# Kernel optimization log

Measured on AMD Instinct MI355X. Metric: run time of the kernel, lower is better.

The kernel has to match this reference:

```python
import jax, jax.numpy as jnp
import numpy as np

HEAD_DIM = 64
SELECT = 256  # number of selected rows/cols (m)
NUM_ITER = 4  # Newton-Schulz iterations


def _select_idx(T, mask, m):
    # top-k over sum of features (select_type='sum'), done under stop_gradient (torch.no_grad)
    somme = jax.lax.stop_gradient(jnp.sum(T, axis=-1))  # [B,H,N]
    neg = -jnp.finfo(somme.dtype).max
    somme = jnp.where(mask[:, None, :], somme, neg)
    _, idx = jax.lax.top_k(somme, m)  # [B,H,m], descending like argsort(descending=True)[:m]
    return idx


def _gather_rows(T, idx):
    # T: [B,H,N,D], idx: [B,H,m] -> [B,H,m,D]  (index_select over flattened (b h n))
    return jnp.take_along_axis(T, idx[..., None], axis=2)


def _iterative_inv(mat, num_iter):
    m = mat.shape[-1]
    I = jnp.eye(m, dtype=mat.dtype)
    K = mat
    # V0 = K^T / max_j(sum_i K_ij)
    scale = 1.0 / jnp.max(jnp.sum(K, axis=-2), axis=-1)[:, :, None, None]
    V = scale * jnp.swapaxes(K, -1, -2)
    for _ in range(num_iter):
        KV = jnp.matmul(K, V)
        V = jnp.matmul(0.25 * V, 13.0 * I - jnp.matmul(KV, 15.0 * I - jnp.matmul(KV, 7.0 * I - KV)))
    return V


def setup_inputs() -> dict:
    key = jax.random.key(0)
    kq, kk, kv = jax.random.split(key, 3)
    B, H, N, D = 2, 8, 4096, HEAD_DIM
    Q = jax.random.normal(kq, (B, H, N, D), dtype=jnp.float32)
    K = jax.random.normal(kk, (B, H, N, D), dtype=jnp.float32)
    V = jax.random.normal(kv, (B, H, N, D), dtype=jnp.float32)
    mask = jnp.ones((B, N), dtype=bool)
    return {"Q": Q, "K": K, "V": V, "mask": mask}


def reference(Q, K, V, mask):
    m = SELECT
    Qs = Q / np.sqrt(HEAD_DIM).astype(np.float32)
    # select_mode='default' -> index_select_different: indices for K from K, for Q from (scaled) Q
    idx_k = _select_idx(K, mask, m)
    idx_q = _select_idx(Qs, mask, m)
    nc = _gather_rows(K, idx_k)   # [B,H,m,D] selected columns (from K)
    nr = _gather_rows(Qs, idx_k := idx_q if False else idx_q) if False else _gather_rows(Qs, idx_q)  # [B,H,m,D]
    c = jnp.einsum('bhnd,bhmd->bhnm', Qs, nc)   # [B,H,N,m]
    r = jnp.einsum('bhmd,bhnd->bhmn', nr, K)    # [B,H,m,N]
    neg = -jnp.finfo(Qs.dtype).max
    r = jnp.where(mask[:, None, None, :], r, neg)
    kernel_1 = jax.nn.softmax(c, axis=-1)                 # [B,H,N,m]
    u = _gather_rows(kernel_1, idx_q)                     # [B,H,m,m]
    kernel_3 = jax.nn.softmax(r, axis=-1)                 # [B,H,m,N]
    kernel_2_inv = _iterative_inv(u, NUM_ITER)            # [B,H,m,m]
    RV = jnp.matmul(kernel_3, V)                          # [B,H,m,D]
    X = jnp.matmul(kernel_1, jnp.matmul(kernel_2_inv, RV))  # [B,H,N,D]
    return X
```

## Files before the change

### kernel.cpp

```cpp
#include <hip/hip_runtime.h>
#include <float.h>


#define G    16
#define NSEQ 4096
#define DH   64
#define MSEL 256
#define NSL  16

typedef __attribute__((ext_vector_type(8))) short short8;
typedef __attribute__((ext_vector_type(4))) float floatx4;
typedef __attribute__((ext_vector_type(4))) unsigned short ushort4v;
typedef unsigned short ush;

static __device__ __forceinline__ ush f2b(float x) {
    union { float f; unsigned u; } c{x};
    unsigned r = c.u + 0x7FFFu + ((c.u >> 16) & 1u);
    return (ush)(r >> 16);
}
static __device__ __forceinline__ float b2f(ush h) {
    union { unsigned u; float f; } c{(unsigned)h << 16};
    return c.f;
}
static __device__ __forceinline__ void split_store(ush* __restrict__ h, ush* __restrict__ l,
                                                   int off, float4 v, float scale) {
    float a0 = v.x * scale, a1 = v.y * scale, a2 = v.z * scale, a3 = v.w * scale;
    ush h0 = f2b(a0), h1 = f2b(a1), h2 = f2b(a2), h3 = f2b(a3);
    ushort4v hv = { h0, h1, h2, h3 };
    ushort4v lv = { f2b(a0 - b2f(h0)), f2b(a1 - b2f(h1)), f2b(a2 - b2f(h2)), f2b(a3 - b2f(h3)) };
    *(ushort4v*)&h[off] = hv;
    *(ushort4v*)&l[off] = lv;
}
static __device__ __forceinline__ floatx4 mfma3(short8 ah, short8 al, short8 bh, short8 bl, floatx4 acc) {
    acc = __builtin_amdgcn_mfma_f32_16x16x32_bf16(al, bh, acc, 0, 0, 0);
    acc = __builtin_amdgcn_mfma_f32_16x16x32_bf16(ah, bl, acc, 0, 0, 0);
    acc = __builtin_amdgcn_mfma_f32_16x16x32_bf16(ah, bh, acc, 0, 0, 0);
    return acc;
}

__global__ __launch_bounds__(256) void rowsum_kernel(const float* __restrict__ Q, const float* __restrict__ K,
                                                     float* __restrict__ sumQ, float* __restrict__ sumK,
                                                     float* __restrict__ k2) {
    long row = (long)blockIdx.x * 16 + (threadIdx.x >> 4);
    int c4 = (threadIdx.x & 15) * 4;
    float4 q = *(const float4*)(Q + row * DH + c4);
    float4 k = *(const float4*)(K + row * DH + c4);
    float qs = q.x + q.y + q.z + q.w;
    float ks = k.x + k.y + k.z + k.w;
    float k2s = k.x * k.x + k.y * k.y + k.z * k.z + k.w * k.w;
#pragma unroll
    for (int off = 8; off; off >>= 1) {
        qs += __shfl_xor(qs, off); ks += __shfl_xor(ks, off); k2s += __shfl_xor(k2s, off);
    }
    if ((threadIdx.x & 15) == 0) { sumQ[row] = qs; sumK[row] = ks; k2[row] = k2s; }
}

__global__ __launch_bounds__(256) void topk_select(const float* __restrict__ sumQ, const float* __restrict__ sumK,
                                                   int* __restrict__ idxQ, int* __restrict__ idxK,
                                                   const float* __restrict__ k2, float* __restrict__ Kmax2,
                                                   float* __restrict__ colsum) {
    __shared__ unsigned red[4];
    __shared__ float redf[4];
    __shared__ unsigned eqpre[64];
    __shared__ unsigned cnt_sel;
    int g = blockIdx.x, which = blockIdx.y;
    const float* s = (which ? sumK : sumQ) + (long)g * NSEQ;
    int* out = (which ? idxK : idxQ) + g * MSEL;
    int t = threadIdx.x, lane = t & 63, wid = t >> 6;
    if (which == 0) colsum[g * 256 + t] = 0.f;
    unsigned k[16];
#pragma unroll
    for (int i = 0; i < 16; i++) {
        unsigned u = __float_as_uint(s[t + 256 * i]);
        k[i] = (u & 0x80000000u) ? ~u : (u | 0x80000000u);
    }
    unsigned T = 0;
    for (int b = 31; b >= 0; b--) {
        unsigned trial = T | (1u << b);
        int c = 0;
#pragma unroll
        for (int i = 0; i < 16; i++) c += (k[i] >= trial);
#pragma unroll
        for (int off = 32; off; off >>= 1) c += __shfl_xor(c, off);
        __syncthreads();
        if (lane == 0) red[wid] = (unsigned)c;
        __syncthreads();
        unsigned tot = red[0] + red[1] + red[2] + red[3];
        if (tot == MSEL) { T = trial; break; }
        if (tot > MSEL) T = trial;
    }
    int cg = 0;
#pragma unroll
    for (int i = 0; i < 16; i++) cg += (k[i] > T);
#pragma unroll
    for (int off = 32; off; off >>= 1) cg += __shfl_xor(cg, off);
    __syncthreads();
    if (lane == 0) red[wid] = (unsigned)cg;
    if (t == 0) cnt_sel = 0;
    __syncthreads();
    unsigned ngreater = red[0] + red[1] + red[2] + red[3];
    unsigned want_eq = MSEL - ngreater;
#pragma unroll
    for (int i = 0; i < 16; i++) {
        unsigned long long be = __ballot(k[i] == T);
        if (lane == 0) eqpre[i * 4 + wid] = (unsigned)__popcll(be);
    }
    __syncthreads();
    if (t == 0) {
        unsigned run = 0;
        for (int j = 0; j < 64; j++) { unsigned c = eqpre[j]; eqpre[j] = run; run += c; }
    }
    __syncthreads();
#pragma unroll
    for (int i = 0; i < 16; i++) {
        int idx = t + 256 * i;
        unsigned long long lt = (1ull << lane) - 1;
        bool gt = (k[i] > T);
        unsigned long long bg = __ballot(gt);
        unsigned wbase = 0;
        if (lane == 0) wbase = atomicAdd(&cnt_sel, (unsigned)__popcll(bg));
        wbase = __shfl((int)wbase, 0);
        if (gt) out[wbase + __popcll(bg & lt)] = idx;
        bool eq = (k[i] == T);
        unsigned long long be = __ballot(eq);
        if (eq) {
            unsigned rank = eqpre[i * 4 + wid] + (unsigned)__popcll(be & lt);
            if (rank < want_eq) out[ngreater + rank] = idx;
        }
    }
    if (which == 1) {
        float mx = 0.f;
#pragma unroll
        for (int i = 0; i < 16; i++) mx = fmaxf(mx, k2[(long)g * NSEQ + t + 256 * i]);
#pragma unroll
        for (int off = 32; off; off >>= 1) mx = fmaxf(mx, __shfl_xor(mx, off));
        __syncthreads();
        if (lane == 0) redf[wid] = mx;
        __syncthreads();
        if (t == 0) Kmax2[g] = fmaxf(fmaxf(redf[0], redf[1]), fmaxf(redf[2], redf[3]));
    }
}

__global__ __launch_bounds__(256) void gather_kernel(const float* __restrict__ Q, const float* __restrict__ K,
                                                     const int* __restrict__ idxQ, const int* __restrict__ idxK,
                                                     const float* __restrict__ Kmax2,
                                                     float* __restrict__ nr,
                                                     ush* __restrict__ ncH, ush* __restrict__ ncL,
                                                     float* __restrict__ Mb) {
    int wid = threadIdx.x >> 6, lane = threadIdx.x & 63;
    long t = (long)blockIdx.x * 4 + wid;
    long g = t >> 8;
    int iq = idxQ[t], ik = idxK[t];
    float qv = Q[(g * NSEQ + iq) * DH + lane] * 0.125f;
    nr[t * DH + lane] = qv;
    float kv = K[(g * NSEQ + ik) * DH + lane];
    ush h = f2b(kv);
    ncH[t * DH + lane] = h;
    ncL[t * DH + lane] = f2b(kv - b2f(h));
    float n2 = qv * qv;
#pragma unroll
    for (int off = 32; off; off >>= 1) n2 += __shfl_xor(n2, off);
    if (lane == 0) Mb[t] = sqrtf(n2 * Kmax2[g]);
}

__global__ __launch_bounds__(256, 4) void flash_rv(const float* __restrict__ nr, const float* __restrict__ K,
                                                   const float* __restrict__ V, const float* __restrict__ Mb,
                                                   float* __restrict__ Lp, float* __restrict__ RVp) {
    __shared__ __align__(16) ush B1h[64 * 72];
    __shared__ __align__(16) ush B1l[64 * 72];
    __shared__ __align__(16) ush Ph[64 * 72];
    __shared__ float msh[64];
    __shared__ float lred[64][2];
    int ns = blockIdx.x, s = blockIdx.y, g = blockIdx.z;
    int t = threadIdx.x, lane = t & 63, w = t >> 6;
    int wr = w >> 1, wc = w & 1, ml = lane & 15, quad = lane >> 4;
    int lr = t >> 2, lq = t & 3;
    const float* nrg = nr + (long)g * 16384 + (long)s * 64 * 64;
    const float* Kg  = K + (long)g * 262144 + (long)ns * 256 * 64;
    const float* Vg  = V + (long)g * 262144 + (long)ns * 256 * 64;
    short8 Ah[2][2], Al[2][2];
// ... 180 lines not shown
    __syncthreads();
    if (MODE == 1) {
        float invL[4][4];
#pragma unroll
        for (int i = 0; i < 4; i++)
#pragma unroll
            for (int r = 0; r < 4; r++) invL[i][r] = 1.0f / Lr[16 * i + quad * 4 + r];
        float* ug = Out + (long)g * 65536 + (long)strip * 64 * 256;
#pragma unroll
        for (int i = 0; i < 4; i++)
#pragma unroll
            for (int r = 0; r < 4; r++) {
                int row = 16 * i + quad * 4 + r;
#pragma unroll
                for (int c = 0; c < 4; c++)
                    ug[(long)row * 256 + c * 64 + w * 16 + ml] = sacc[c][i][r] * invL[i][r];
            }
#pragma unroll
        for (int c = 0; c < 4; c++) {
            float v = 0.f;
#pragma unroll
            for (int i = 0; i < 4; i++)
#pragma unroll
                for (int r = 0; r < 4; r++) v += sacc[c][i][r] * invL[i][r];
            v += __shfl_xor(v, 16);
            v += __shfl_xor(v, 32);
            if (quad == 0) atomicAdd(&colsum[g * 256 + c * 64 + w * 16 + ml], v);
        }
        return;
    }
    floatx4 xacc[2][2] = {};
    const ush* wHg = WtH + (long)g * 16384;
    const ush* wLg = WtL + (long)g * 16384;
#pragma unroll
    for (int h = 0; h < 4; h++) {
        __syncthreads();
#pragma unroll
        for (int i = 0; i < 4; i++)
#pragma unroll
            for (int r = 0; r < 4; r++) {
                int row = 16 * i + quad * 4 + r;
                float p = sacc[h][i][r];
                ush hh = f2b(p);
                Ph[row * 72 + w * 16 + ml] = hh;
                Pl[row * 72 + w * 16 + ml] = f2b(p - b2f(hh));
            }
        {
            const ush* sH = wHg + lr * 256 + h * 64;
            const ush* sL = wLg + lr * 256 + h * 64;
            *(uint4*)&Wh[lr * 72 + lq * 8]       = *(const uint4*)&sH[lq * 8];
            *(uint4*)&Wh[lr * 72 + (lq + 4) * 8] = *(const uint4*)&sH[(lq + 4) * 8];
            *(uint4*)&Wl[lr * 72 + lq * 8]       = *(const uint4*)&sL[lq * 8];
            *(uint4*)&Wl[lr * 72 + (lq + 4) * 8] = *(const uint4*)&sL[(lq + 4) * 8];
        }
        __syncthreads();
#pragma unroll
        for (int kq = 0; kq < 2; kq++) {
            short8 a0h = *(const short8*)&Ph[(wr * 32 + ml) * 72 + kq * 32 + quad * 8];
            short8 a0l = *(const short8*)&Pl[(wr * 32 + ml) * 72 + kq * 32 + quad * 8];
            short8 a1h = *(const short8*)&Ph[(wr * 32 + 16 + ml) * 72 + kq * 32 + quad * 8];
            short8 a1l = *(const short8*)&Pl[(wr * 32 + 16 + ml) * 72 + kq * 32 + quad * 8];
            short8 b0h = *(const short8*)&Wh[(wc * 32 + ml) * 72 + kq * 32 + quad * 8];
            short8 b0l = *(const short8*)&Wl[(wc * 32 + ml) * 72 + kq * 32 + quad * 8];
            short8 b1h = *(const short8*)&Wh[(wc * 32 + 16 + ml) * 72 + kq * 32 + quad * 8];
            short8 b1l = *(const short8*)&Wl[(wc * 32 + 16 + ml) * 72 + kq * 32 + quad * 8];
            xacc[0][0] = mfma3(a0h, a0l, b0h, b0l, xacc[0][0]);
            xacc[0][1] = mfma3(a0h, a0l, b1h, b1l, xacc[0][1]);
            xacc[1][0] = mfma3(a1h, a1l, b0h, b0l, xacc[1][0]);
            xacc[1][1] = mfma3(a1h, a1l, b1h, b1l, xacc[1][1]);
        }
    }
    float* outg = Out + (long)g * 262144 + (long)strip * 64 * 64;
#pragma unroll
    for (int i2 = 0; i2 < 2; i2++)
#pragma unroll
        for (int j2 = 0; j2 < 2; j2++)
#pragma unroll
            for (int r = 0; r < 4; r++) {
                int row = wr * 32 + i2 * 16 + quad * 4 + r;
                outg[(long)row * 64 + wc * 32 + j2 * 16 + ml] = xacc[i2][j2][r] / Lr[row];
            }
}

__global__ __launch_bounds__(256) void mergeprep_kernel(const float* __restrict__ Lp, const float* __restrict__ RVp,
                                                        ush* __restrict__ RVt,
                                                        const float* __restrict__ u, const float* __restrict__ colsum,
                                                        ush* __restrict__ u_bf, ush* __restrict__ V0,
                                                        float* __restrict__ scale) {
    __shared__ float tile[64][65];
    __shared__ float smax[4];
    int g = blockIdx.y;
    int t = threadIdx.x, lane = t & 63, wid = t >> 6;
    if (blockIdx.z == 0) {
        int s = blockIdx.x >> 2, mq = blockIdx.x & 3;
        int d = t & 63;
        int m0 = mq * 16 + (t >> 6) * 4;
        long pb = ((long)(g * 4 + s)) * NSL;
#pragma unroll
        for (int mm = 0; mm < 4; mm++) {
            int rho = m0 + mm;
            float L = 0.f, val = 0.f;
#pragma unroll
            for (int n = 0; n < NSL; n++) {
                L   += Lp[(pb + n) * 64 + rho];
                val += RVp[(pb + n) * 4096 + rho * 64 + d];
            }
            RVt[(long)g * 16384 + d * 256 + s * 64 + rho] = f2b(val / L);
        }
        return;
    }
    int tc = blockIdx.x & 3, tr = (blockIdx.x >> 2) & 3;
    float v = colsum[g * 256 + t];
#pragma unroll
    for (int off = 32; off; off >>= 1) v = fmaxf(v, __shfl_xor(v, off));
    if (lane == 0) smax[wid] = v;
    __syncthreads();
    float sc = 1.0f / fmaxf(fmaxf(smax[0], smax[1]), fmaxf(smax[2], smax[3]));
    if (t == 0 && tr == 0 && tc == 0) scale[g] = sc;
    long base = (long)g * MSEL * MSEL;
    const float* ug = u + base;
    int cq = (t & 15) * 4, r0 = t >> 4;
#pragma unroll
    for (int i = 0; i < 4; i++) {
        int r = r0 + 16 * i;
        float4 vv = *(const float4*)&ug[(long)(tr * 64 + r) * MSEL + tc * 64 + cq];
        long o = base + (long)(tr * 64 + r) * MSEL + tc * 64 + cq;
        ushort4v ub = { f2b(vv.x), f2b(vv.y), f2b(vv.z), f2b(vv.w) };
        *(ushort4v*)&u_bf[o] = ub;
        tile[r][cq] = vv.x; tile[r][cq + 1] = vv.y; tile[r][cq + 2] = vv.z; tile[r][cq + 3] = vv.w;
    }
    __syncthreads();
#pragma unroll
    for (int i = 0; i < 4; i++) {
        int r = r0 + 16 * i;
        ushort4v o = { f2b(sc * tile[cq][r]), f2b(sc * tile[cq + 1][r]),
                       f2b(sc * tile[cq + 2][r]), f2b(sc * tile[cq + 3][r]) };
        *(ushort4v*)&V0[base + (long)(tc * 64 + r) * MSEL + tr * 64 + cq] = o;
    }
}

__global__ __launch_bounds__(256) void nsAC(const ush* __restrict__ A0, const ush* __restrict__ B0t,
                                            const ush* __restrict__ A1, const ush* __restrict__ B1t,
                                            ush* __restrict__ C0rm, ush* __restrict__ C0t,
                                            ush* __restrict__ C1rm,
                                            const float* __restrict__ scale, int whichBase) {
    const int LD = 136;
    __shared__ __align__(16) ush As[64 * LD];
    __shared__ __align__(16) ush Bs[64 * LD];
    int z = blockIdx.z, g = z & 15, which = (z >> 4) + whichBase;
    int tm = blockIdx.y, tn = blockIdx.x;
    long base = (long)g * 65536;
    const ush* Ag = (which ? A1 : A0) + base + (long)tm * 64 * 256;
    const ush* Bg = (which ? B1t : B0t) + base + (long)tn * 64 * 256;
    int t = threadIdx.x;
    int lr = t >> 2, lq = t & 3;
    int w = t >> 6, lane = t & 63;
    int wr = w >> 1, wc = w & 1;
    int ml = lane & 15, quad = lane >> 4;
    floatx4 acc[2][2] = {};
#pragma unroll
    for (int h = 0; h < 2; h++) {
        __syncthreads();
#pragma unroll
        for (int rr = 0; rr < 4; rr++) {
            int col = (lq + 4 * rr) * 8;
            *(uint4*)&As[lr * LD + col] = *(const uint4*)(Ag + lr * 256 + h * 128 + col);
            *(uint4*)&Bs[lr * LD + col] = *(const uint4*)(Bg + lr * 256 + h * 128 + col);
        }
        __syncthreads();
#pragma unroll
        for (int kq = 0; kq < 4; kq++) {
            int ko = kq * 32 + quad * 8;
            short8 a0 = *(const short8*)&As[(wr * 32 + ml) * LD + ko];
            short8 a1 = *(const short8*)&As[(wr * 32 + 16 + ml) * LD + ko];
            short8 b0 = *(const short8*)&Bs[(wc * 32 + ml) * LD + ko];
            short8 b1 = *(const short8*)&Bs[(wc * 32 + 16 + ml) * LD + ko];
            acc[0][0] = __builtin_amdgcn_mfma_f32_16x16x32_bf16(a0, b0, acc[0][0], 0, 0, 0);
            acc[0][1] = __builtin_amdgcn_mfma_f32_16x16x32_bf16(a0, b1, acc[0][1], 0, 0, 0);
            acc[1][0] = __builtin_amdgcn_mfma_f32_16x16x32_bf16(a1, b0, acc[1][0], 0, 0, 0);
            acc[1][1] = __builtin_amdgcn_mfma_f32_16x16x32_bf16(a1, b1, acc[1][1], 0, 0, 0);
        }
    }
    float sc = (which == 0 && scale) ? scale[g] : 1.0f;
    int rowb = tm * 64 + wr * 32, colb = tn * 64 + wc * 32;
#pragma unroll
    for (int i = 0; i < 2; i++) {
#pragma unroll
        for (int j = 0; j < 2; j++) {
            int col = colb + j * 16 + ml;
            int r0 = rowb + i * 16 + quad * 4;
            ush h[4];
#pragma unroll
            for (int r = 0; r < 4; r++) h[r] = f2b(acc[i][j][r] * sc);
            if (which == 0) {
#pragma unroll
                for (int r = 0; r < 4; r++) C0rm[base + (long)(r0 + r) * 256 + col] = h[r];
                ushort4v ht = { h[0], h[1], h[2], h[3] };
                *(ushort4v*)&C0t[base + (long)col * 256 + r0] = ht;
            } else {
#pragma unroll
                for (int r = 0; r < 4; r++) C1rm[base + (long)(r0 + r) * 256 + col] = h[r];
            }
        }
    }
}

template <bool FINAL>
__global__ __launch_bounds__(256) void nsB(const ush* __restrict__ S, const ush* __restrict__ Et,
                                           const ush* __restrict__ St,
                                           ush* __restrict__ Eo, ush* __restrict__ Eot,
                                           ush* __restrict__ Pt) {
    const int LD = 136;
    __shared__ __align__(16) ush As[64 * LD];
    __shared__ __align__(16) ush B1s[64 * LD];
    __shared__ __align__(16) ush B2s[64 * LD];
    int g = blockIdx.z, tm = blockIdx.y, tn = blockIdx.x;
    long base = (long)g * 65536;
    const ush* Ag  = S + base + (long)tm * 64 * 256;
    const ush* B1g = Et + base + (long)tn * 64 * 256;
    const ush* B2g = St + base + (long)tn * 64 * 256;
    int t = threadIdx.x;
    int lr = t >> 2, lq = t & 3;
    int w = t >> 6, lane = t & 63;
    int wr = w >> 1, wc = w & 1;
    int ml = lane & 15, quad = lane >> 4;
    floatx4 acc1[2][2] = {};
    floatx4 acc2[2][2] = {};
#pragma unroll
    for (int h = 0; h < 2; h++) {
        __syncthreads();
#pragma unroll
        for (int rr = 0; rr < 4; rr++) {
            int col = (lq + 4 * rr) * 8;
            *(uint4*)&As[lr * LD + col]  = *(const uint4*)(Ag + lr * 256 + h * 128 + col);
            *(uint4*)&B1s[lr * LD + col] = *(const uint4*)(B1g + lr * 256 + h * 128 + col);
            if (!FINAL) *(uint4*)&B2s[lr * LD + col] = *(const uint4*)(B2g + lr * 256 + h * 128 + col);
        }
        __syncthreads();
#pragma unroll
        for (int kq = 0; kq < 4; kq++) {
            int ko = kq * 32 + quad * 8;
            short8 a0 = *(const short8*)&As[(wr * 32 + ml) * LD + ko];
            short8 a1 = *(const short8*)&As[(wr * 32 + 16 + ml) * LD + ko];
            short8 b10 = *(const short8*)&B1s[(wc * 32 + ml) * LD + ko];
            short8 b11 = *(const short8*)&B1s[(wc * 32 + 16 + ml) * LD + ko];
            acc1[0][0] = __builtin_amdgcn_mfma_f32_16x16x32_bf16(a0, b10, acc1[0][0], 0, 0, 0);
            acc1[0][1] = __builtin_amdgcn_mfma_f32_16x16x32_bf16(a0, b11, acc1[0][1], 0, 0, 0);
            acc1[1][0] = __builtin_amdgcn_mfma_f32_16x16x32_bf16(a1, b10, acc1[1][0], 0, 0, 0);
            acc1[1][1] = __builtin_amdgcn_mfma_f32_16x16x32_bf16(a1, b11, acc1[1][1], 0, 0, 0);
            if (!FINAL) {
                short8 b20 = *(const short8*)&B2s[(wc * 32 + ml) * LD + ko];
                short8 b21 = *(const short8*)&B2s[(wc * 32 + 16 + ml) * LD + ko];
                acc2[0][0] = __builtin_amdgcn_mfma_f32_16x16x32_bf16(a0, b20, acc2[0][0], 0, 0, 0);
                acc2[0][1] = __builtin_amdgcn_mfma_f32_16x16x32_bf16(a0, b21, acc2[0][1], 0, 0, 0);
                acc2[1][0] = __builtin_amdgcn_mfma_f32_16x16x32_bf16(a1, b20, acc2[1][0], 0, 0, 0);
                acc2[1][1] = __builtin_amdgcn_mfma_f32_16x16x32_bf16(a1, b21, acc2[1][1], 0, 0, 0);
            }
        }
    }
    int rowb = tm * 64 + wr * 32, colb = tn * 64 + wc * 32;
#pragma unroll
    for (int i = 0; i < 2; i++) {
#pragma unroll
        for (int j = 0; j < 2; j++) {
            int col = colb + j * 16 + ml;
            int r0 = rowb + i * 16 + quad * 4;
            ushort4v et = *(const ushort4v*)&Et[base + (long)col * 256 + r0];
            ushort4v st = *(const ushort4v*)&St[base + (long)col * 256 + r0];
            ushort4v pv;
#pragma unroll
            for (int r = 0; r < 4; r++) {
                float e = b2f(et[r]), s = b2f(st[r]);
                float p = 0.25f * (((r0 + r == col) ? 13.0f : 0.0f) - 15.0f * e + 7.0f * s - acc1[i][j][r]);
                pv[r] = f2b(p);
            }
            *(ushort4v*)&Pt[base + (long)col * 256 + r0] = pv;
            if (!FINAL) {
                ush h[4];
#pragma unroll
                for (int r = 0; r < 4; r++) {
                    float e = b2f(et[r]), s = b2f(st[r]);
                    float en = 0.25f * (13.0f * e - 15.0f * s + 7.0f * acc1[i][j][r] - acc2[i][j][r]);
                    h[r] = f2b(en);
                }
#pragma unroll
                for (int r = 0; r < 4; r++) Eo[base + (long)(r0 + r) * 256 + col] = h[r];
                ushort4v ht = { h[0], h[1], h[2], h[3] };
                *(ushort4v*)&Eot[base + (long)col * 256 + r0] = ht;
            }
        }
    }
}

__global__ __launch_bounds__(256) void nsW(const ush* __restrict__ V4, const ush* __restrict__ RVt,
                                           ush* __restrict__ WtH, ush* __restrict__ WtL) {
    const int LD = 136;
    __shared__ __align__(16) ush As[64 * LD];
    __shared__ __align__(16) ush Bs[64 * LD];
    int g = blockIdx.z, tm = blockIdx.y;
    long base = (long)g * 65536;
    const ush* Ag = V4 + base + (long)tm * 64 * 256;
    const ush* Bg = RVt + (long)g * 16384;
    int t = threadIdx.x;
    int lr = t >> 2, lq = t & 3;
    int w = t >> 6, lane = t & 63;
    int wr = w >> 1, wc = w & 1;
    int ml = lane & 15, quad = lane >> 4;
    floatx4 acc[2][2] = {};
#pragma unroll
    for (int h = 0; h < 2; h++) {
        __syncthreads();
#pragma unroll
        for (int rr = 0; rr < 4; rr++) {
            int col = (lq + 4 * rr) * 8;
            *(uint4*)&As[lr * LD + col] = *(const uint4*)(Ag + lr * 256 + h * 128 + col);
            *(uint4*)&Bs[lr * LD + col] = *(const uint4*)(Bg + lr * 256 + h * 128 + col);
        }
        __syncthreads();
#pragma unroll
        for (int kq = 0; kq < 4; kq++) {
            int ko = kq * 32 + quad * 8;
            short8 a0 = *(const short8*)&As[(wr * 32 + ml) * LD + ko];
            short8 a1 = *(const short8*)&As[(wr * 32 + 16 + ml) * LD + ko];
            short8 b0 = *(const short8*)&Bs[(wc * 32 + ml) * LD + ko];
            short8 b1 = *(const short8*)&Bs[(wc * 32 + 16 + ml) * LD + ko];
            acc[0][0] = __builtin_amdgcn_mfma_f32_16x16x32_bf16(a0, b0, acc[0][0], 0, 0, 0);
            acc[0][1] = __builtin_amdgcn_mfma_f32_16x16x32_bf16(a0, b1, acc[0][1], 0, 0, 0);
            acc[1][0] = __builtin_amdgcn_mfma_f32_16x16x32_bf16(a1, b0, acc[1][0], 0, 0, 0);
            acc[1][1] = __builtin_amdgcn_mfma_f32_16x16x32_bf16(a1, b1, acc[1][1], 0, 0, 0);
        }
    }
    int rowb = tm * 64 + wr * 32, colb = wc * 32;
#pragma unroll
    for (int i = 0; i < 2; i++) {
#pragma unroll
        for (int j = 0; j < 2; j++) {
            int col = colb + j * 16 + ml;
            int r0 = rowb + i * 16 + quad * 4;
            ushort4v hv, lv;
#pragma unroll
            for (int r = 0; r < 4; r++) {
                float v = acc[i][j][r];
                ush h = f2b(v);
                hv[r] = h;
                lv[r] = f2b(v - b2f(h));
            }
            *(ushort4v*)&WtH[(long)g * 16384 + (long)col * 256 + r0] = hv;
            *(ushort4v*)&WtL[(long)g * 16384 + (long)col * 256 + r0] = lv;
        }
    }
}

extern "C" void kernel_launch(void* const* d_in, const int* in_sizes, int n_in,
                              void* d_out, int out_size, void* d_ws, size_t ws_size,
                              hipStream_t stream) {
    (void)in_sizes; (void)n_in; (void)out_size; (void)ws_size;
    const float* Q = (const float*)d_in[0];
    const float* K = (const float*)d_in[1];
    const float* V = (const float*)d_in[2];

    float* ws    = (float*)d_ws;
    float* sumQ  = ws;
    float* sumK  = sumQ + 65536;
    float* k2    = sumK + 65536;
    float* nr    = k2 + 65536;
    float* u     = nr + 262144;
    float* Mb    = u + 1048576;
    float* Kmax2 = Mb + 4096;
    float* scale = Kmax2 + 16;
    float* colsum= scale + 16 + 32;
    float* Lp    = colsum + 4096;
    float* RVp   = Lp + 65536;
    int* idxQ    = (int*)(RVp + 4194304);
    int* idxK    = idxQ + 4096;
    ush* ncH     = (ush*)(idxK + 4096);
    ush* ncL     = ncH + 262144;
    ush* WtH     = ncL + 262144;
    ush* WtL     = WtH + 262144;
    ush* RVt     = WtL + 262144;
    ush* u_bf    = RVt + 262144;
    ush* Vacc_a  = u_bf + 1048576;
    ush* Vacc_b  = Vacc_a + 1048576;
    ush* E_a     = Vacc_b + 1048576;
    ush* Et_a    = E_a + 1048576;
    ush* E_b     = Et_a + 1048576;
    ush* Et_b    = E_b + 1048576;
    ush* Sbuf    = Et_b + 1048576;
    ush* St      = Sbuf + 1048576;
    ush* Ptb     = St + 1048576;

    dim3 blk(256);

    hipLaunchKernelGGL(rowsum_kernel, dim3(G * NSEQ / 16), blk, 0, stream, Q, K, sumQ, sumK, k2);
    hipLaunchKernelGGL(topk_select, dim3(G, 2), blk, 0, stream, sumQ, sumK, idxQ, idxK, k2, Kmax2, colsum);
    hipLaunchKernelGGL(gather_kernel, dim3(G * MSEL / 4), blk, 0, stream, Q, K, idxQ, idxK, Kmax2, nr, ncH, ncL, Mb);

    hipLaunchKernelGGL(flash_rv, dim3(NSL, 4, G), blk, 0, stream, nr, K, V, Mb, Lp, RVp);

    hipLaunchKernelGGL((fused_cx<1>), dim3(4, G), blk, 0, stream, nr, ncH, ncL,
                       (const ush*)0, (const ush*)0, u, colsum, 1.0f);

    hipLaunchKernelGGL(mergeprep_kernel, dim3(16, G, 2), blk, 0, stream,
                       Lp, RVp, RVt, u, colsum, u_bf, Vacc_a, scale);

    hipLaunchKernelGGL(nsAC, dim3(4, 4, G), blk, 0, stream,
                       u_bf, u_bf, (const ush*)0, (const ush*)0, E_a, Et_a, (ush*)0, scale, 0);
    hipLaunchKernelGGL(nsAC, dim3(4, 4, G), blk, 0, stream,
                       E_a, Et_a, (const ush*)0, (const ush*)0, Sbuf, St, (ush*)0, (const float*)0, 0);

    ush* E = E_a;  ush* Et = Et_a;
    ush* En = E_b; ush* Ent = Et_b;
    ush* Vc = Vacc_a; ush* Vn = Vacc_b;
    for (int i = 0; i < 3; i++) {
        hipLaunchKernelGGL((nsB<false>), dim3(4, 4, G), blk, 0, stream, Sbuf, Et, St, En, Ent, Ptb);
        hipLaunchKernelGGL(nsAC, dim3(4, 4, 2 * G), blk, 0, stream,
                           En, Ent, Vc, Ptb, Sbuf, St, Vn, (const float*)0, 0);
        ush* tp;
        tp = E; E = En; En = tp;
        tp = Et; Et = Ent; Ent = tp;
        tp = Vc; Vc = Vn; Vn = tp;
    }
    hipLaunchKernelGGL((nsB<true>), dim3(4, 4, G), blk, 0, stream, Sbuf, Et, St, (ush*)0, (ush*)0, Ptb);
    hipLaunchKernelGGL(nsAC, dim3(4, 4, G), blk, 0, stream,
                       (const ush*)0, (const ush*)0, Vc, Ptb, (ush*)0, (ush*)0, Vn, (const float*)0, 1);
    hipLaunchKernelGGL(nsW, dim3(1, 4, G), blk, 0, stream, Vn, RVt, WtH, WtL);

    hipLaunchKernelGGL((fused_cx<0>), dim3(64, G), blk, 0, stream, Q, ncH, ncL, WtH, WtL,
                       (float*)d_out, (float*)0, 0.125f);
}
```

Baseline: 255.3 us.

## Fuse Newton-Schulz inverse chain into one cooperative kernel with grid syncs

Replaces the chain of mergeprep, nsAC, nsB and nsW launches (about 12 kernels) with a single cooperative kernel of 256 blocks that runs every stage in sequence, separated by grid.sync(). It targets per-launch overhead and inter-kernel gaps in the small 256x256 Newton-Schulz matmuls. In exchange it pays for grid-wide barriers, and in the 2x-split nsAC stages each block now does both matmuls serially where two separate blocks used to run them. It also depends on all 256 blocks being co-resident.

```diff
diff --git a/kernel.cpp b/kernel.cpp
--- a/kernel.cpp
+++ b/kernel.cpp
@@ -1,4 +1,5 @@
 #include <hip/hip_runtime.h>
+#include <hip/hip_cooperative_groups.h>
 #include <float.h>
 
 
@@ -7,6 +8,8 @@
 #define DH   64
 #define MSEL 256
 #define NSL  16
+
+namespace cg = cooperative_groups;
 
 typedef __attribute__((ext_vector_type(8))) short short8;
 typedef __attribute__((ext_vector_type(4))) float floatx4;
@@ -89,13 +92,13 @@
         if (tot == MSEL) { T = trial; break; }
         if (tot > MSEL) T = trial;
     }
-    int cg = 0;
-#pragma unroll
-    for (int i = 0; i < 16; i++) cg += (k[i] > T);
-#pragma unroll
-    for (int off = 32; off; off >>= 1) cg += __shfl_xor(cg, off);
+    int cg2 = 0;
+#pragma unroll
+    for (int i = 0; i < 16; i++) cg2 += (k[i] > T);
+#pragma unroll
+    for (int off = 32; off; off >>= 1) cg2 += __shfl_xor(cg2, off);
     __syncthreads();
-    if (lane == 0) red[wid] = (unsigned)cg;
+    if (lane == 0) red[wid] = (unsigned)cg2;
     if (t == 0) cnt_sel = 0;
     __syncthreads();
     unsigned ngreater = red[0] + red[1] + red[2] + red[3];
@@ -442,109 +445,67 @@
             }
 }
 
-__global__ __launch_bounds__(256) void mergeprep_kernel(const float* __restrict__ Lp, const float* __restrict__ RVp,
-                                                        ush* __restrict__ RVt,
-                                                        const float* __restrict__ u, const float* __restrict__ colsum,
-                                                        ush* __restrict__ u_bf, ush* __restrict__ V0,
-                                                        float* __restrict__ scale) {
-    __shared__ float tile[64][65];
-    __shared__ float smax[4];
-    int g = blockIdx.y;
-    int t = threadIdx.x, lane = t & 63, wid = t >> 6;
-    if (blockIdx.z == 0) {
-        int s = blockIdx.x >> 2, mq = blockIdx.x & 3;
-        int d = t & 63;
-        int m0 = mq * 16 + (t >> 6) * 4;
-        long pb = ((long)(g * 4 + s)) * NSL;
-#pragma unroll
-        for (int mm = 0; mm < 4; mm++) {
-            int rho = m0 + mm;
-            float L = 0.f, val = 0.f;
-#pragma unroll
-            for (int n = 0; n < NSL; n++) {
-                L   += Lp[(pb + n) * 64 + rho];
-                val += RVp[(pb + n) * 4096 + rho * 64 + d];
-            }
-            RVt[(long)g * 16384 + d * 256 + s * 64 + rho] = f2b(val / L);
-        }
-        return;
-    }
-    int tc = blockIdx.x & 3, tr = (blockIdx.x >> 2) & 3;
-    float v = colsum[g * 256 + t];
-#pragma unroll
-    for (int off = 32; off; off >>= 1) v = fmaxf(v, __shfl_xor(v, off));
-    if (lane == 0) smax[wid] = v;
-    __syncthreads();
-    float sc = 1.0f / fmaxf(fmaxf(smax[0], smax[1]), fmaxf(smax[2], smax[3]));
-    if (t == 0 && tr == 0 && tc == 0) scale[g] = sc;
-    long base = (long)g * MSEL * MSEL;
-    const float* ug = u + base;
-    int cq = (t & 15) * 4, r0 = t >> 4;
-#pragma unroll
-    for (int i = 0; i < 4; i++) {
-        int r = r0 + 16 * i;
-        float4 vv = *(const float4*)&ug[(long)(tr * 64 + r) * MSEL + tc * 64 + cq];
-        long o = base + (long)(tr * 64 + r) * MSEL + tc * 64 + cq;
-        ushort4v ub = { f2b(vv.x), f2b(vv.y), f2b(vv.z), f2b(vv.w) };
-        *(ushort4v*)&u_bf[o] = ub;
-        tile[r][cq] = vv.x; tile[r][cq + 1] = vv.y; tile[r][cq + 2] = vv.z; tile[r][cq + 3] = vv.w;
-    }
-    __syncthreads();
-#pragma unroll
-    for (int i = 0; i < 4; i++) {
-        int r = r0 + 16 * i;
-        ushort4v o = { f2b(sc * tile[cq][r]), f2b(sc * tile[cq + 1][r]),
-                       f2b(sc * tile[cq + 2][r]), f2b(sc * tile[cq + 3][r]) };
-        *(ushort4v*)&V0[base + (long)(tc * 64 + r) * MSEL + tr * 64 + cq] = o;
-    }
-}
-
-__global__ __launch_bounds__(256) void nsAC(const ush* __restrict__ A0, const ush* __restrict__ B0t,
-                                            const ush* __restrict__ A1, const ush* __restrict__ B1t,
-                                            ush* __restrict__ C0rm, ush* __restrict__ C0t,
-                                            ush* __restrict__ C1rm,
-                                            const float* __restrict__ scale, int whichBase) {
-    const int LD = 136;
-    __shared__ __align__(16) ush As[64 * LD];
-    __shared__ __align__(16) ush Bs[64 * LD];
-    int z = blockIdx.z, g = z & 15, which = (z >> 4) + whichBase;
-    int tm = blockIdx.y, tn = blockIdx.x;
-    long base = (long)g * 65536;
-    const ush* Ag = (which ? A1 : A0) + base + (long)tm * 64 * 256;
-    const ush* Bg = (which ? B1t : B0t) + base + (long)tn * 64 * 256;
-    int t = threadIdx.x;
+struct NSArgs {
+    const float* Lp; const float* RVp; ush* RVt;
+    const float* u; const float* colsum;
+    ush* u_bf; float* scale;
+    ush* Va; ush* Vb;
+    ush* E_a; ush* Et_a; ush* E_b; ush* Et_b;
+    ush* S; ush* St; ush* Pt;
+    ush* WtH; ush* WtL;
+};
+
+#define NSLD 136
+
+template <bool DUAL>
+static __device__ __forceinline__ void mm_core(const ush* __restrict__ Ag, const ush* __restrict__ B1g,
+                                               const ush* __restrict__ B2g,
+                                               ush* As, ush* B1s, ush* B2s,
+                                               floatx4 (&acc1)[2][2], floatx4 (&acc2)[2][2], int t) {
     int lr = t >> 2, lq = t & 3;
     int w = t >> 6, lane = t & 63;
-    int wr = w >> 1, wc = w & 1;
-    int ml = lane & 15, quad = lane >> 4;
-    floatx4 acc[2][2] = {};
+    int wr = w >> 1, wc = w & 1, ml = lane & 15, quad = lane >> 4;
 #pragma unroll
     for (int h = 0; h < 2; h++) {
         __syncthreads();
 #pragma unroll
         for (int rr = 0; rr < 4; rr++) {
             int col = (lq + 4 * rr) * 8;
-            *(uint4*)&As[lr * LD + col] = *(const uint4*)(Ag + lr * 256 + h * 128 + col);
-            *(uint4*)&Bs[lr * LD + col] = *(const uint4*)(Bg + lr * 256 + h * 128 + col);
+            *(uint4*)&As[lr * NSLD + col]  = *(const uint4*)(Ag + lr * 256 + h * 128 + col);
+            *(uint4*)&B1s[lr * NSLD + col] = *(const uint4*)(B1g + lr * 256 + h * 128 + col);
+            if (DUAL) *(uint4*)&B2s[lr * NSLD + col] = *(const uint4*)(B2g + lr * 256 + h * 128 + col);
         }
         __syncthreads();
 #pragma unroll
         for (int kq = 0; kq < 4; kq++) {
             int ko = kq * 32 + quad * 8;
-            short8 a0 = *(const short8*)&As[(wr * 32 + ml) * LD + ko];
-            short8 a1 = *(const short8*)&As[(wr * 32 + 16 + ml) * LD + ko];
-            short8 b0 = *(const short8*)&Bs[(wc * 32 + ml) * LD + ko];
-            short8 b1 = *(const short8*)&Bs[(wc * 32 + 16 + ml) * LD + ko];
-            acc[0][0] = __builtin_amdgcn_mfma_f32_16x16x32_bf16(a0, b0, acc[0][0], 0, 0, 0);
-            acc[0][1] = __builtin_amdgcn_mfma_f32_16x16x32_bf16(a0, b1, acc[0][1], 0, 0, 0);
-            acc[1][0] = __builtin_amdgcn_mfma_f32_16x16x32_bf16(a1, b0, acc[1][0], 0, 0, 0);
-            acc[1][1] = __builtin_amdgcn_mfma_f32_16x16x32_bf16(a1, b1, acc[1][1], 0, 0, 0);
-        }
-    }
-    float sc = (which == 0 && scale) ? scale[g] : 1.0f;
+            short8 a0 = *(const short8*)&As[(wr * 32 + ml) * NSLD + ko];
+            short8 a1 = *(const short8*)&As[(wr * 32 + 16 + ml) * NSLD + ko];
+            short8 b10 = *(const short8*)&B1s[(wc * 32 + ml) * NSLD + ko];
+            short8 b11 = *(const short8*)&B1s[(wc * 32 + 16 + ml) * NSLD + ko];
+            acc1[0][0] = __builtin_amdgcn_mfma_f32_16x16x32_bf16(a0, b10, acc1[0][0], 0, 0, 0);
+            acc1[0][1] = __builtin_amdgcn_mfma_f32_16x16x32_bf16(a0, b11, acc1[0][1], 0, 0, 0);
+            acc1[1][0] = __builtin_amdgcn_mfma_f32_16x16x32_bf16(a1, b10, acc1[1][0], 0, 0, 0);
+            acc1[1][1] = __builtin_amdgcn_mfma_f32_16x16x32_bf16(a1, b11, acc1[1][1], 0, 0, 0);
+            if (DUAL) {
+                short8 b20 = *(const short8*)&B2s[(wc * 32 + ml) * NSLD + ko];
+                short8 b21 = *(const short8*)&B2s[(wc * 32 + 16 + ml) * NSLD + ko];
+                acc2[0][0] = __builtin_amdgcn_mfma_f32_16x16x32_bf16(a0, b20, acc2[0][0], 0, 0, 0);
+                acc2[0][1] = __builtin_amdgcn_mfma_f32_16x16x32_bf16(a0, b21, acc2[0][1], 0, 0, 0);
+                acc2[1][0] = __builtin_amdgcn_mfma_f32_16x16x32_bf16(a1, b20, acc2[1][0], 0, 0, 0);
+                acc2[1][1] = __builtin_amdgcn_mfma_f32_16x16x32_bf16(a1, b21, acc2[1][1], 0, 0, 0);
+            }
+        }
+    }
+}
+
+static __device__ __forceinline__ void ep_rm_t(ush* __restrict__ rm, ush* __restrict__ tr, long base,
+                                               int tm, int tn, floatx4 (&acc)[2][2], float sc, int t) {
+    int w = t >> 6, lane = t & 63;
+    int wr = w >> 1, wc = w & 1, ml = lane & 15, quad = lane >> 4;
     int rowb = tm * 64 + wr * 32, colb = tn * 64 + wc * 32;
 #pragma unroll
-    for (int i = 0; i < 2; i++) {
+    for (int i = 0; i < 2; i++)
 #pragma unroll
         for (int j = 0; j < 2; j++) {
             int col = colb + j * 16 + ml;
@@ -552,162 +513,242 @@
             ush h[4];
 #pragma unroll
             for (int r = 0; r < 4; r++) h[r] = f2b(acc[i][j][r] * sc);
-            if (which == 0) {
-#pragma unroll
-                for (int r = 0; r < 4; r++) C0rm[base + (long)(r0 + r) * 256 + col] = h[r];
-                ushort4v ht = { h[0], h[1], h[2], h[3] };
-                *(ushort4v*)&C0t[base + (long)col * 256 + r0] = ht;
-            } else {
-#pragma unroll
-                for (int r = 0; r < 4; r++) C1rm[base + (long)(r0 + r) * 256 + col] = h[r];
-            }
-        }
-    }
-}
-
-template <bool FINAL>
-__global__ __launch_bounds__(256) void nsB(const ush* __restrict__ S, const ush* __restrict__ Et,
-                                           const ush* __restrict__ St,
-                                           ush* __restrict__ Eo, ush* __restrict__ Eot,
-                                           ush* __restrict__ Pt) {
-    const int LD = 136;
-    __shared__ __align__(16) ush As[64 * LD];
-    __shared__ __align__(16) ush B1s[64 * LD];
-    __shared__ __align__(16) ush B2s[64 * LD];
-    int g = blockIdx.z, tm = blockIdx.y, tn = blockIdx.x;
+#pragma unroll
+            for (int r = 0; r < 4; r++) rm[base + (long)(r0 + r) * 256 + col] = h[r];
+            ushort4v ht = { h[0], h[1], h[2], h[3] };
+            *(ushort4v*)&tr[base + (long)col * 256 + r0] = ht;
+        }
+}
+
+__global__ __launch_bounds__(256, 1) void ns_mega(NSArgs a) {
+    __shared__ __align__(16) ush SM[3 * 64 * NSLD];
+    ush* As  = SM;
+    ush* B1s = SM + 64 * NSLD;
+    ush* B2s = SM + 2 * 64 * NSLD;
+    cg::grid_group grid = cg::this_grid();
+    int b = blockIdx.x;
+    int t = threadIdx.x, lane = t & 63, wid = t >> 6;
+    int g = b >> 4, tile = b & 15, tm = tile >> 2, tn = tile & 3;
     long base = (long)g * 65536;
-    const ush* Ag  = S + base + (long)tm * 64 * 256;
-    const ush* B1g = Et + base + (long)tn * 64 * 256;
-    const ush* B2g = St + base + (long)tn * 64 * 256;
-    int t = threadIdx.x;
-    int lr = t >> 2, lq = t & 3;
-    int w = t >> 6, lane = t & 63;
-    int wr = w >> 1, wc = w & 1;
-    int ml = lane & 15, quad = lane >> 4;
-    floatx4 acc1[2][2] = {};
-    floatx4 acc2[2][2] = {};
-#pragma unroll
-    for (int h = 0; h < 2; h++) {
-        __syncthreads();
-#pragma unroll
-        for (int rr = 0; rr < 4; rr++) {
-            int col = (lq + 4 * rr) * 8;
-            *(uint4*)&As[lr * LD + col]  = *(const uint4*)(Ag + lr * 256 + h * 128 + col);
-            *(uint4*)&B1s[lr * LD + col] = *(const uint4*)(B1g + lr * 256 + h * 128 + col);
-            if (!FINAL) *(uint4*)&B2s[lr * LD + col] = *(const uint4*)(B2g + lr * 256 + h * 128 + col);
-        }
-        __syncthreads();
-#pragma unroll
-        for (int kq = 0; kq < 4; kq++) {
-            int ko = kq * 32 + quad * 8;
-            short8 a0 = *(const short8*)&As[(wr * 32 + ml) * LD + ko];
-            short8 a1 = *(const short8*)&As[(wr * 32 + 16 + ml) * LD + ko];
-            short8 b10 = *(const short8*)&B1s[(wc * 32 + ml) * LD + ko];
-            short8 b11 = *(const short8*)&B1s[(wc * 32 + 16 + ml) * LD + ko];
-            acc1[0][0] = __builtin_amdgcn_mfma_f32_16x16x32_bf16(a0, b10, acc1[0][0], 0, 0, 0);
-            acc1[0][1] = __builtin_amdgcn_mfma_f32_16x16x32_bf16(a0, b11, acc1[0][1], 0, 0, 0);
-            acc1[1][0] = __builtin_amdgcn_mfma_f32_16x16x32_bf16(a1, b10, acc1[1][0], 0, 0, 0);
-            acc1[1][1] = __builtin_amdgcn_mfma_f32_16x16x32_bf16(a1, b11, acc1[1][1], 0, 0, 0);
-            if (!FINAL) {
-                short8 b20 = *(const short8*)&B2s[(wc * 32 + ml) * LD + ko];
-                short8 b21 = *(const short8*)&B2s[(wc * 32 + 16 + ml) * LD + ko];
-                acc2[0][0] = __builtin_amdgcn_mfma_f32_16x16x32_bf16(a0, b20, acc2[0][0], 0, 0, 0);
-                acc2[0][1] = __builtin_amdgcn_mfma_f32_16x16x32_bf16(a0, b21, acc2[0][1], 0, 0, 0);
-                acc2[1][0] = __builtin_amdgcn_mfma_f32_16x16x32_bf16(a1, b20, acc2[1][0], 0, 0, 0);
-                acc2[1][1] = __builtin_amdgcn_mfma_f32_16x16x32_bf16(a1, b21, acc2[1][1], 0, 0, 0);
-            }
-        }
-    }
-    int rowb = tm * 64 + wr * 32, colb = tn * 64 + wc * 32;
-#pragma unroll
-    for (int i = 0; i < 2; i++) {
-#pragma unroll
-        for (int j = 0; j < 2; j++) {
-            int col = colb + j * 16 + ml;
-            int r0 = rowb + i * 16 + quad * 4;
-            ushort4v et = *(const ushort4v*)&Et[base + (long)col * 256 + r0];
-            ushort4v st = *(const ushort4v*)&St[base + (long)col * 256 + r0];
-            ushort4v pv;
-#pragma unroll
-            for (int r = 0; r < 4; r++) {
-                float e = b2f(et[r]), s = b2f(st[r]);
-                float p = 0.25f * (((r0 + r == col) ? 13.0f : 0.0f) - 15.0f * e + 7.0f * s - acc1[i][j][r]);
-                pv[r] = f2b(p);
-            }
-            *(ushort4v*)&Pt[base + (long)col * 256 + r0] = pv;
-            if (!FINAL) {
-                ush h[4];
+    floatx4 acc1[2][2], acc2[2][2];
+
+    {
+        int s = tile >> 2, mq = tile & 3;
+        int d = t & 63;
+        int m0 = mq * 16 + (t >> 6) * 4;
+        long pb = ((long)(g * 4 + s)) * NSL;
+#pragma unroll
+        for (int mm = 0; mm < 4; mm++) {
+            int rho = m0 + mm;
+            float L = 0.f, val = 0.f;
+#pragma unroll
+            for (int n = 0; n < NSL; n++) {
+                L   += a.Lp[(pb + n) * 64 + rho];
+                val += a.RVp[(pb + n) * 4096 + (long)rho * 64 + d];
+            }
+            a.RVt[(long)g * 16384 + d * 256 + s * 64 + rho] = f2b(val / L);
+        }
+        int tc = tile & 3, tr = tile >> 2;
+        float* ftile = (float*)SM;
+        float* smax  = (float*)(SM + 2 * 64 * NSLD);
+        float v = a.colsum[g * 256 + t];
+#pragma unroll
+        for (int off = 32; off; off >>= 1) v = fmaxf(v, __shfl_xor(v, off));
+        if (lane == 0) smax[wid] = v;
+        __syncthreads();
+        float sc = 1.0f / fmaxf(fmaxf(smax[0], smax[1]), fmaxf(smax[2], smax[3]));
+        if (t == 0 && tile == 0) a.scale[g] = sc;
+        const float* ug = a.u + base;
+        int cq = (t & 15) * 4, r0 = t >> 4;
+#pragma unroll
+        for (int i = 0; i < 4; i++) {
+            int r = r0 + 16 * i;
+            float4 vv = *(const float4*)&ug[(long)(tr * 64 + r) * MSEL + tc * 64 + cq];
+            long o = base + (long)(tr * 64 + r) * MSEL + tc * 64 + cq;
+            ushort4v ub = { f2b(vv.x), f2b(vv.y), f2b(vv.z), f2b(vv.w) };
+            *(ushort4v*)&a.u_bf[o] = ub;
+            ftile[r * 65 + cq] = vv.x; ftile[r * 65 + cq + 1] = vv.y;
+            ftile[r * 65 + cq + 2] = vv.z; ftile[r * 65 + cq + 3] = vv.w;
+        }
+        __syncthreads();
+#pragma unroll
+        for (int i = 0; i < 4; i++) {
+            int r = r0 + 16 * i;
+            ushort4v o = { f2b(sc * ftile[cq * 65 + r]), f2b(sc * ftile[(cq + 1) * 65 + r]),
+                           f2b(sc * ftile[(cq + 2) * 65 + r]), f2b(sc * ftile[(cq + 3) * 65 + r]) };
+            *(ushort4v*)&a.Va[base + (long)(tc * 64 + r) * MSEL + tr * 64 + cq] = o;
+        }
+    }
+    grid.sync();
+
+    {
+#pragma unroll
+        for (int i = 0; i < 2; i++)
+#pragma unroll
+            for (int j = 0; j < 2; j++) acc1[i][j] = floatx4{0.f, 0.f, 0.f, 0.f};
+        mm_core<false>(a.u_bf + base + (long)tm * 64 * 256, a.u_bf + base + (long)tn * 64 * 256,
+                       (const ush*)0, As, B1s, B2s, acc1, acc2, t);
+        ep_rm_t(a.E_a, a.Et_a, base, tm, tn, acc1, a.scale[g], t);
+    }
+    grid.sync();
+
+    {
+#pragma unroll
+        for (int i = 0; i < 2; i++)
+#pragma unroll
+            for (int j = 0; j < 2; j++) acc1[i][j] = floatx4{0.f, 0.f, 0.f, 0.f};
+        mm_core<false>(a.E_a + base + (long)tm * 64 * 256, a.Et_a + base + (long)tn * 64 * 256,
+                       (const ush*)0, As, B1s, B2s, acc1, acc2, t);
+        ep_rm_t(a.S, a.St, base, tm, tn, acc1, 1.0f, t);
+    }
+    grid.sync();
+
+    ush* E = a.E_a;  ush* Et = a.Et_a;
+    ush* En = a.E_b; ush* Ent = a.Et_b;
+    ush* Vc = a.Va;  ush* Vn = a.Vb;
+    int w = t >> 6;
+    int wr = w >> 1, wc = w & 1, ml = lane & 15, quad = lane >> 4;
+    for (int it = 0; it < 3; it++) {
+#pragma unroll
+        for (int i = 0; i < 2; i++)
+#pragma unroll
+            for (int j = 0; j < 2; j++) { acc1[i][j] = floatx4{0.f,0.f,0.f,0.f}; acc2[i][j] = floatx4{0.f,0.f,0.f,0.f}; }
+        mm_core<true>(a.S + base + (long)tm * 64 * 256, Et + base + (long)tn * 64 * 256,
+                      a.St + base + (long)tn * 64 * 256, As, B1s, B2s, acc1, acc2, t);
+        {
+            int rowb = tm * 64 + wr * 32, colb = tn * 64 + wc * 32;
+#pragma unroll
+            for (int i = 0; i < 2; i++)
+#pragma unroll
+                for (int j = 0; j < 2; j++) {
+                    int col = colb + j * 16 + ml;
+                    int r0 = rowb + i * 16 + quad * 4;
+                    ushort4v et = *(const ushort4v*)&Et[base + (long)col * 256 + r0];
+                    ushort4v st = *(const ushort4v*)&a.St[base + (long)col * 256 + r0];
+                    ushort4v pv;
+                    ush h[4];
+#pragma unroll
+                    for (int r = 0; r < 4; r++) {
+                        float e = b2f(et[r]), s = b2f(st[r]);
+                        float p = 0.25f * (((r0 + r == col) ? 13.0f : 0.0f) - 15.0f * e + 7.0f * s - acc1[i][j][r]);
+                        pv[r] = f2b(p);
+                        float en = 0.25f * (13.0f * e - 15.0f * s + 7.0f * acc1[i][j][r] - acc2[i][j][r]);
+                        h[r] = f2b(en);
+                    }
+                    *(ushort4v*)&a.Pt[base + (long)col * 256 + r0] = pv;
+#pragma unroll
+                    for (int r = 0; r < 4; r++) En[base + (long)(r0 + r) * 256 + col] = h[r];
+                    ushort4v ht = { h[0], h[1], h[2], h[3] };
+                    *(ushort4v*)&Ent[base + (long)col * 256 + r0] = ht;
+                }
+        }
+        grid.sync();
+#pragma unroll
+        for (int i = 0; i < 2; i++)
+#pragma unroll
+            for (int j = 0; j < 2; j++) acc1[i][j] = floatx4{0.f,0.f,0.f,0.f};
+        mm_core<false>(En + base + (long)tm * 64 * 256, Ent + base + (long)tn * 64 * 256,
+                       (const ush*)0, As, B1s, B2s, acc1, acc2, t);
+        ep_rm_t(a.S, a.St, base, tm, tn, acc1, 1.0f, t);
+#pragma unroll
+        for (int i = 0; i < 2; i++)
+#pragma unroll
+            for (int j = 0; j < 2; j++) acc1[i][j] = floatx4{0.f,0.f,0.f,0.f};
+        mm_core<false>(Vc + base + (long)tm * 64 * 256, a.Pt + base + (long)tn * 64 * 256,
+                       (const ush*)0, As, B1s, B2s, acc1, acc2, t);
+        {
+            int rowb = tm * 64 + wr * 32, colb = tn * 64 + wc * 32;
+#pragma unroll
+            for (int i = 0; i < 2; i++)
+#pragma unroll
+                for (int j = 0; j < 2; j++) {
+                    int col = colb + j * 16 + ml;
+                    int r0 = rowb + i * 16 + quad * 4;
+#pragma unroll
+                    for (int r = 0; r < 4; r++) Vn[base + (long)(r0 + r) * 256 + col] = f2b(acc1[i][j][r]);
+                }
+        }
+        grid.sync();
+        ush* tp;
+        tp = E; E = En; En = tp;
+        tp = Et; Et = Ent; Ent = tp;
+        tp = Vc; Vc = Vn; Vn = tp;
+    }
+
+    {
+#pragma unroll
+        for (int i = 0; i < 2; i++)
+#pragma unroll
+            for (int j = 0; j < 2; j++) acc1[i][j] = floatx4{0.f,0.f,0.f,0.f};
+        mm_core<false>(a.S + base + (long)tm * 64 * 256, Et + base + (long)tn * 64 * 256,
+                       (const ush*)0, As, B1s, B2s, acc1, acc2, t);
+        int rowb = tm * 64 + wr * 32, colb = tn * 64 + wc * 32;
+#pragma unroll
+        for (int i = 0; i < 2; i++)
+#pragma unroll
+            for (int j = 0; j < 2; j++) {
+                int col = colb + j * 16 + ml;
+                int r0 = rowb + i * 16 + quad * 4;
+                ushort4v et = *(const ushort4v*)&Et[base + (long)col * 256 + r0];
+                ushort4v st = *(const ushort4v*)&a.St[base + (long)col * 256 + r0];
+                ushort4v pv;
 #pragma unroll
                 for (int r = 0; r < 4; r++) {
                     float e = b2f(et[r]), s = b2f(st[r]);
-                    float en = 0.25f * (13.0f * e - 15.0f * s + 7.0f * acc1[i][j][r] - acc2[i][j][r]);
-                    h[r] = f2b(en);
+                    pv[r] = f2b(0.25f * (((r0 + r == col) ? 13.0f : 0.0f) - 15.0f * e + 7.0f * s - acc1[i][j][r]));
                 }
-#pragma unroll
-                for (int r = 0; r < 4; r++) Eo[base + (long)(r0 + r) * 256 + col] = h[r];
-                ushort4v ht = { h[0], h[1], h[2], h[3] };
-                *(ushort4v*)&Eot[base + (long)col * 256 + r0] = ht;
-            }
-        }
-    }
-}
-
-__global__ __launch_bounds__(256) void nsW(const ush* __restrict__ V4, const ush* __restrict__ RVt,
-                                           ush* __restrict__ WtH, ush* __restrict__ WtL) {
-    const int LD = 136;
-    __shared__ __align__(16) ush As[64 * LD];
-    __shared__ __align__(16) ush Bs[64 * LD];
-    int g = blockIdx.z, tm = blockIdx.y;
-    long base = (long)g * 65536;
-    const ush* Ag = V4 + base + (long)tm * 64 * 256;
-    const ush* Bg = RVt + (long)g * 16384;
-    int t = threadIdx.x;
-    int lr = t >> 2, lq = t & 3;
-    int w = t >> 6, lane = t & 63;
-    int wr = w >> 1, wc = w & 1;
-    int ml = lane & 15, quad = lane >> 4;
-    floatx4 acc[2][2] = {};
-#pragma unroll
-    for (int h = 0; h < 2; h++) {
-        __syncthreads();
-#pragma unroll
-        for (int rr = 0; rr < 4; rr++) {
-            int col = (lq + 4 * rr) * 8;
-            *(uint4*)&As[lr * LD + col] = *(const uint4*)(Ag + lr * 256 + h * 128 + col);
-            *(uint4*)&Bs[lr * LD + col] = *(const uint4*)(Bg + lr * 256 + h * 128 + col);
-        }
-        __syncthreads();
-#pragma unroll
-        for (int kq = 0; kq < 4; kq++) {
-            int ko = kq * 32 + quad * 8;
-            short8 a0 = *(const short8*)&As[(wr * 32 + ml) * LD + ko];
-            short8 a1 = *(const short8*)&As[(wr * 32 + 16 + ml) * LD + ko];
-            short8 b0 = *(const short8*)&Bs[(wc * 32 + ml) * LD + ko];
-            short8 b1 = *(const short8*)&Bs[(wc * 32 + 16 + ml) * LD + ko];
-            acc[0][0] = __builtin_amdgcn_mfma_f32_16x16x32_bf16(a0, b0, acc[0][0], 0, 0, 0);
-            acc[0][1] = __builtin_amdgcn_mfma_f32_16x16x32_bf16(a0, b1, acc[0][1], 0, 0, 0);
-            acc[1][0] = __builtin_amdgcn_mfma_f32_16x16x32_bf16(a1, b0, acc[1][0], 0, 0, 0);
-            acc[1][1] = __builtin_amdgcn_mfma_f32_16x16x32_bf16(a1, b1, acc[1][1], 0, 0, 0);
-        }
-    }
-    int rowb = tm * 64 + wr * 32, colb = wc * 32;
-#pragma unroll
-    for (int i = 0; i < 2; i++) {
-#pragma unroll
-        for (int j = 0; j < 2; j++) {
-            int col = colb + j * 16 + ml;
-            int r0 = rowb + i * 16 + quad * 4;
-            ushort4v hv, lv;
-#pragma unroll
-            for (int r = 0; r < 4; r++) {
-                float v = acc[i][j][r];
-                ush h = f2b(v);
-                hv[r] = h;
-                lv[r] = f2b(v - b2f(h));
-            }
-            *(ushort4v*)&WtH[(long)g * 16384 + (long)col * 256 + r0] = hv;
-            *(ushort4v*)&WtL[(long)g * 16384 + (long)col * 256 + r0] = lv;
-        }
+                *(ushort4v*)&a.Pt[base + (long)col * 256 + r0] = pv;
+            }
+    }
+    grid.sync();
+
+    {
+#pragma unroll
+        for (int i = 0; i < 2; i++)
+#pragma unroll
+            for (int j = 0; j < 2; j++) acc1[i][j] = floatx4{0.f,0.f,0.f,0.f};
+        mm_core<false>(Vc + base + (long)tm * 64 * 256, a.Pt + base + (long)tn * 64 * 256,
+                       (const ush*)0, As, B1s, B2s, acc1, acc2, t);
+        int rowb = tm * 64 + wr * 32, colb = tn * 64 + wc * 32;
+#pragma unroll
+        for (int i = 0; i < 2; i++)
+#pragma unroll
+            for (int j = 0; j < 2; j++) {
+                int col = colb + j * 16 + ml;
+                int r0 = rowb + i * 16 + quad * 4;
+#pragma unroll
+                for (int r = 0; r < 4; r++) Vn[base + (long)(r0 + r) * 256 + col] = f2b(acc1[i][j][r]);
+            }
+    }
+    grid.sync();
+
+    if (b < 64) {
+        int gw = b >> 2, tmw = b & 3;
+        long bw = (long)gw * 65536;
+#pragma unroll
+        for (int i = 0; i < 2; i++)
+#pragma unroll
+            for (int j = 0; j < 2; j++) acc1[i][j] = floatx4{0.f,0.f,0.f,0.f};
+        mm_core<false>(Vn + bw + (long)tmw * 64 * 256, a.RVt + (long)gw * 16384,
+                       (const ush*)0, As, B1s, B2s, acc1, acc2, t);
+        int rowb = tmw * 64 + wr * 32, colb = wc * 32;
+#pragma unroll
+        for (int i = 0; i < 2; i++)
+#pragma unroll
+            for (int j = 0; j < 2; j++) {
+                int col = colb + j * 16 + ml;
+                int r0 = rowb + i * 16 + quad * 4;
+                ushort4v hv, lv;
+#pragma unroll
+                for (int r = 0; r < 4; r++) {
+                    float v = acc1[i][j][r];
+                    ush h = f2b(v);
+                    hv[r] = h;
+                    lv[r] = f2b(v - b2f(h));
+                }
+                *(ushort4v*)&a.WtH[(long)gw * 16384 + (long)col * 256 + r0] = hv;
+                *(ushort4v*)&a.WtL[(long)gw * 16384 + (long)col * 256 + r0] = lv;
+            }
     }
 }
 
@@ -760,30 +801,16 @@
     hipLaunchKernelGGL((fused_cx<1>), dim3(4, G), blk, 0, stream, nr, ncH, ncL,
                        (const ush*)0, (const ush*)0, u, colsum, 1.0f);
 
-    hipLaunchKernelGGL(mergeprep_kernel, dim3(16, G, 2), blk, 0, stream,
-                       Lp, RVp, RVt, u, colsum, u_bf, Vacc_a, scale);
-
-    hipLaunchKernelGGL(nsAC, dim3(4, 4, G), blk, 0, stream,
-                       u_bf, u_bf, (const ush*)0, (const ush*)0, E_a, Et_a, (ush*)0, scale, 0);
-    hipLaunchKernelGGL(nsAC, dim3(4, 4, G), blk, 0, stream,
-                       E_a, Et_a, (const ush*)0, (const ush*)0, Sbuf, St, (ush*)0, (const float*)0, 0);
-
-    ush* E = E_a;  ush* Et = Et_a;
-    ush* En = E_b; ush* Ent = Et_b;
-    ush* Vc = Vacc_a; ush* Vn = Vacc_b;
-    for (int i = 0; i < 3; i++) {
-        hipLaunchKernelGGL((nsB<false>), dim3(4, 4, G), blk, 0, stream, Sbuf, Et, St, En, Ent, Ptb);
-        hipLaunchKernelGGL(nsAC, dim3(4, 4, 2 * G), blk, 0, stream,
-                           En, Ent, Vc, Ptb, Sbuf, St, Vn, (const float*)0, 0);
-        ush* tp;
-        tp = E; E = En; En = tp;
-        tp = Et; Et = Ent; Ent = tp;
-        tp = Vc; Vc = Vn; Vn = tp;
-    }
-    hipLaunchKernelGGL((nsB<true>), dim3(4, 4, G), blk, 0, stream, Sbuf, Et, St, (ush*)0, (ush*)0, Ptb);
-    hipLaunchKernelGGL(nsAC, dim3(4, 4, G), blk, 0, stream,
-                       (const ush*)0, (const ush*)0, Vc, Ptb, (ush*)0, (ush*)0, Vn, (const float*)0, 1);
-    hipLaunchKernelGGL(nsW, dim3(1, 4, G), blk, 0, stream, Vn, RVt, WtH, WtL);
+    NSArgs nsa;
+    nsa.Lp = Lp; nsa.RVp = RVp; nsa.RVt = RVt;
+    nsa.u = u; nsa.colsum = colsum;
+    nsa.u_bf = u_bf; nsa.scale = scale;
+    nsa.Va = Vacc_a; nsa.Vb = Vacc_b;
+    nsa.E_a = E_a; nsa.Et_a = Et_a; nsa.E_b = E_b; nsa.Et_b = Et_b;
+    nsa.S = Sbuf; nsa.St = St; nsa.Pt = Ptb;
+    nsa.WtH = WtH; nsa.WtL = WtL;
+    void* kargs[] = { (void*)&nsa };
+    hipLaunchCooperativeKernel((const void*)ns_mega, dim3(256), dim3(256), kargs, 0, stream);
 
     hipLaunchKernelGGL((fused_cx<0>), dim3(64, G), blk, 0, stream, Q, ncH, ncL, WtH, WtL,
                        (float*)d_out, (float*)0, 0.125f);
```

Result: slower. 616.6 us (+141.5%).
